# Kernel optimization log

Hardware: AMD Instinct MI355X
Metric: run time of the kernel (lower is better)

The kernel has to match this reference:

```python
import jax, jax.numpy as jnp
import numpy as np

N = 100000       # nodes
E = 1600000      # edges (avg degree 16)
F_IN = 20        # NUM_FEATURES
H = 128          # hidden_channels
EPS = 1e-5       # GraphNorm eps


def setup_inputs() -> dict:
    key = jax.random.key(0)
    ks = jax.random.split(key, 24)
    s = 0.05
    inp = {
        "x": jax.random.normal(ks[0], (N, F_IN), jnp.float32),
        "edge_index": jax.random.randint(ks[1], (2, E), 0, N, dtype=jnp.int32),
    }
    # SAGEConv params: lin_l (neighbors, with bias), lin_r (root, no bias)
    dims = [(F_IN, H), (H, H), (H, H)]
    k = 2
    for i, (din, dout) in enumerate(dims):
        inp[f"Wl{i}"] = jax.random.normal(ks[k], (dout, din), jnp.float32) * s; k += 1
        inp[f"bl{i}"] = jnp.zeros((dout,), jnp.float32)
        inp[f"Wr{i}"] = jax.random.normal(ks[k], (dout, din), jnp.float32) * s; k += 1
        # GraphNorm: weight, bias, mean_scale (alpha)
        inp[f"gw{i}"] = jnp.ones((dout,), jnp.float32)
        inp[f"gb{i}"] = jnp.zeros((dout,), jnp.float32)
        inp[f"ga{i}"] = jnp.ones((dout,), jnp.float32)
    # MLP head: 128 -> 64 -> 32 -> 1
    inp["hW1"] = jax.random.normal(ks[k], (64, H), jnp.float32) * s; k += 1
    inp["hb1"] = jnp.zeros((64,), jnp.float32)
    inp["hW2"] = jax.random.normal(ks[k], (32, 64), jnp.float32) * s; k += 1
    inp["hb2"] = jnp.zeros((32,), jnp.float32)
    inp["hW3"] = jax.random.normal(ks[k], (1, 32), jnp.float32) * s; k += 1
    inp["hb3"] = jnp.zeros((1,), jnp.float32)
    return inp


def _sage(x, src, dst, Wl, bl, Wr):
    # mean aggregation of source features at destination nodes
    deg = jax.ops.segment_sum(jnp.ones((src.shape[0],), x.dtype), dst, num_segments=N)
    agg = jax.ops.segment_sum(x[src], dst, num_segments=N)
    agg = agg / jnp.maximum(deg, 1.0)[:, None]
    return agg @ Wl.T + bl + x @ Wr.T


def _graphnorm(x, w, b, a):
    # single graph (batch=None): stats over all nodes, per channel
    mean = jnp.mean(x, axis=0)
    c = x - a * mean
    var = jnp.mean(c * c, axis=0)
    return w * c * jax.lax.rsqrt(var + EPS) + b


def reference(x, edge_index,
              Wl0, bl0, Wr0, gw0, gb0, ga0,
              Wl1, bl1, Wr1, gw1, gb1, ga1,
              Wl2, bl2, Wr2, gw2, gb2, ga2,
              hW1, hb1, hW2, hb2, hW3, hb3):
    src, dst = edge_index[0], edge_index[1]
    layers = [(Wl0, bl0, Wr0, gw0, gb0, ga0),
              (Wl1, bl1, Wr1, gw1, gb1, ga1),
              (Wl2, bl2, Wr2, gw2, gb2, ga2)]
    h = x
    for (Wl, bl, Wr, gw, gb, ga) in layers:
        h = _sage(h, src, dst, Wl, bl, Wr)
        h = _graphnorm(h, gw, gb, ga)
        h = jax.nn.gelu(h, approximate=False)  # dropout: eval mode (identity)
    h = jax.nn.gelu(h @ hW1.T + hb1, approximate=False)
    h = jax.nn.gelu(h @ hW2.T + hb2, approximate=False)
    out = jax.nn.sigmoid(h @ hW3.T + hb3)
    return out.squeeze(-1)  # [N]
```

## Files before the change

### kernel.cpp

```cpp
#include <hip/hip_runtime.h>
#include <hip/hip_bf16.h>
#include <math.h>

#define NN 100000
#define EE 1600000
#define FIN 20
#define HH 128
#define NBUK 391
#define FILLB 196
#define MMB 782

typedef __attribute__((ext_vector_type(8))) short bf16x8;
typedef __attribute__((ext_vector_type(4))) float f32x4;

__device__ __forceinline__ unsigned short f2b(float x) {
    unsigned int b = __float_as_uint(x);
    unsigned int r = b + 0x7fffu + ((b >> 16) & 1u);
    return (unsigned short)(r >> 16);
}
__device__ __forceinline__ float lof(unsigned int u) { return __uint_as_float(u << 16); }
__device__ __forceinline__ float hif(unsigned int u) { return __uint_as_float(u & 0xffff0000u); }
__device__ __forceinline__ unsigned int pk2(float a, float b) {
    return (unsigned int)f2b(a) | ((unsigned int)f2b(b) << 16);
}

__device__ __forceinline__ float gelu_exact(float z) {
    return 0.5f * z * (1.0f + erff(z * 0.70710678118654752f));
}

__global__ __launch_bounds__(256) void kb_cnt(const int* __restrict__ dst,
                                              int* __restrict__ bcnt) {
    __shared__ int c[NBUK];
    int t = threadIdx.x;
    for (int i = t; i < NBUK; i += 256) c[i] = 0;
    __syncthreads();
    int e0 = blockIdx.x * 8192;
    #pragma unroll 4
    for (int i = 0; i < 32; ++i) {
        int e = e0 + i * 256 + t;
        if (e < EE) atomicAdd(&c[dst[e] >> 8], 1);
    }
    __syncthreads();
    for (int i = t; i < NBUK; i += 256) if (c[i]) atomicAdd(&bcnt[i], c[i]);
}

__global__ void kb_scan(const int* __restrict__ bcnt, int* __restrict__ bbase,
                        int* __restrict__ cursor) {
    __shared__ int sh[512];
    int t = threadIdx.x;
    int v = (t < NBUK) ? bcnt[t] : 0;
    sh[t] = v;
    __syncthreads();
    for (int off = 1; off < 512; off <<= 1) {
        int add = (t >= off) ? sh[t - off] : 0;
        __syncthreads();
        sh[t] += add;
        __syncthreads();
    }
    if (t < NBUK) {
        int ex = sh[t] - v;
        bbase[t] = ex;
        cursor[t] = ex;
    }
    if (t == NBUK - 1) bbase[NBUK] = sh[t];
}

__global__ __launch_bounds__(256) void kb_fill(const int* __restrict__ src,
        const int* __restrict__ dst, int* __restrict__ cursor,
        unsigned int* __restrict__ pairs) {
    __shared__ int cnt[NBUK], base[NBUK], boff[NBUK];
    int t = threadIdx.x;
    for (int i = t; i < NBUK; i += 256) { cnt[i] = 0; boff[i] = 0; }
    __syncthreads();
    int e0 = blockIdx.x * 8192;
    #pragma unroll 4
    for (int i = 0; i < 32; ++i) {
        int e = e0 + i * 256 + t;
        if (e < EE) atomicAdd(&cnt[dst[e] >> 8], 1);
    }
    __syncthreads();
    for (int i = t; i < NBUK; i += 256)
        if (cnt[i]) base[i] = atomicAdd(&cursor[i], cnt[i]);
    __syncthreads();
    #pragma unroll 4
    for (int i = 0; i < 32; ++i) {
        int e = e0 + i * 256 + t;
        if (e < EE) {
            int d = dst[e];
            int b = d >> 8;
            int pos = base[b] + atomicAdd(&boff[b], 1);
            pairs[pos] = (unsigned int)src[e] | ((unsigned int)(d & 255) << 17);
        }
    }
}

__global__ __launch_bounds__(256) void kb_csr(const unsigned int* __restrict__ pairs,
        const int* __restrict__ bbase, int* __restrict__ row_start,
        int* __restrict__ deg, float* __restrict__ invdeg, int* __restrict__ col) {
    __shared__ int ldeg[256];
    __shared__ int lcnt[256];
    int b = blockIdx.x, t = threadIdx.x;
    int e0 = bbase[b], e1 = bbase[b + 1];
    ldeg[t] = 0;
    lcnt[t] = 0;
    __syncthreads();
    for (int e = e0 + t; e < e1; e += 256) atomicAdd(&ldeg[pairs[e] >> 17], 1);
    __syncthreads();
    int d = ldeg[t];
    for (int off = 1; off < 256; off <<= 1) {
        int add = (t >= off) ? ldeg[t - off] : 0;
        __syncthreads();
        ldeg[t] += add;
        __syncthreads();
    }
    int n = b * 256 + t;
    if (n < NN) {
        row_start[n] = e0 + ldeg[t] - d;
        deg[n] = d;
        invdeg[n] = 1.0f / fmaxf((float)d, 1.0f);
    }
    __syncthreads();
    for (int e = e0 + t; e < e1; e += 256) {
        unsigned int p = pairs[e];
        int dL = p >> 17;
        int pos = e0 + (dL ? ldeg[dL - 1] : 0) + atomicAdd(&lcnt[dL], 1);
        col[pos] = (int)(p & 0x1FFFFu);
    }
}

#define XB_N  (NN * 32)
#define A0_N  (NN * 64)
#define PACK_TOTAL (XB_N + A0_N + 8192 + 32768 + 32768 + 8192 + 2048 + 64 + 32 + NBUK)
__global__ __launch_bounds__(256) void k_pack_all(const float* __restrict__ x,
        const float* __restrict__ Wl0, const float* __restrict__ Wr0,
        const float* __restrict__ Wl1, const float* __restrict__ Wr1,
        const float* __restrict__ Wl2, const float* __restrict__ Wr2,
        const float* __restrict__ hW1, const float* __restrict__ hW2,
        const float* __restrict__ hb1, const float* __restrict__ hb2,
        unsigned short* __restrict__ xb, unsigned short* __restrict__ A0,
        unsigned short* __restrict__ Wt0, unsigned short* __restrict__ Wt2a,
        unsigned short* __restrict__ Wt2b, unsigned short* __restrict__ W1b,
        unsigned short* __restrict__ W2b, float* __restrict__ bH1,
        float* __restrict__ bH2, int* __restrict__ bcnt) {
    int id = blockIdx.x * 256 + threadIdx.x;
    if (id < XB_N) {
        int n = id >> 5, k = id & 31;
        xb[id] = f2b((k < FIN) ? x[n * FIN + k] : 0.0f);
        return;
    }
    id -= XB_N;
    if (id < A0_N) {
        int k = id & 63;
        if (k >= FIN) {
            int n = id >> 6;
            float v = (k >= 32 && k < 32 + FIN) ? x[n * FIN + (k - 32)] : 0.0f;
            A0[id] = f2b(v);
        }
        return;
    }
    id -= A0_N;
    if (id < 8192) {
        int c = id >> 6, k = id & 63;
        float v = 0.0f;
        if (k < FIN) v = Wl0[c * FIN + k];
        else if (k >= 32 && k < 32 + FIN) v = Wr0[c * FIN + (k - 32)];
        Wt0[id] = f2b(v);
        return;
    }
    id -= 8192;
    if (id < 32768) {
        int c = id >> 8, k = id & 255;
        Wt2a[id] = f2b((k < HH) ? Wl1[c * HH + k] : Wr1[c * HH + (k - HH)]);
        return;
    }
    id -= 32768;
    if (id < 32768) {
        int c = id >> 8, k = id & 255;
        Wt2b[id] = f2b((k < HH) ? Wl2[c * HH + k] : Wr2[c * HH + (k - HH)]);
        return;
    }
    id -= 32768;
    if (id < 8192) { W1b[id] = f2b(hW1[id]); return; }
    id -= 8192;
    if (id < 2048) { W2b[id] = f2b(hW2[id]); return; }
    id -= 2048;
    if (id < 64) { bH1[id] = hb1[id]; return; }
    id -= 64;
    if (id < 32) { bH2[id] = hb2[id]; return; }
    id -= 32;
    if (id < NBUK) { bcnt[id] = 0; return; }
}

__global__ __launch_bounds__(256) void k_agg0(const uint2* __restrict__ xb2,
        const int* __restrict__ rs, const int* __restrict__ deg,
        const float* __restrict__ inv, const int* __restrict__ col,
        unsigned short* __restrict__ A0) {
    int wid = threadIdx.x >> 6;
    int lane = threadIdx.x & 63;
    int er = lane >> 3;
    int c8 = lane & 7;
    int n = blockIdx.x * 4 + wid;
    if (n >= NN) return;
    int s = rs[n], d = deg[n];
    float a0 = 0.f, a1 = 0.f, a2 = 0.f, a3 = 0.f;
    for (int j0 = 0; j0 < d; j0 += 8) {
        int j = j0 + er;
        if (j < d) {
            int c = col[s + j];
            uint2 v = xb2[(size_t)c * 8 + c8];
            a0 += lof(v.x); a1 += hif(v.x);
            a2 += lof(v.y); a3 += hif(v.y);
        }
    }
    #pragma unroll
    for (int m = 8; m < 64; m <<= 1) {
        a0 += __shfl_xor(a0, m, 64);
        a1 += __shfl_xor(a1, m, 64);
        a2 += __shfl_xor(a2, m, 64);
        a3 += __shfl_xor(a3, m, 64);
    }
    if (er == 0 && c8 < 5) {
        float iv = inv[n];
        uint2 o;
        o.x = pk2(a0 * iv, a1 * iv);
        o.y = pk2(a2 * iv, a3 * iv);
        ((uint2*)A0)[(size_t)n * 16 + c8] = o;
    }
}

__global__ __launch_bounds__(64) void k_aggb(const unsigned short* __restrict__ hB,
        const int* __restrict__ rs, const int* __restrict__ deg,
        const float* __restrict__ inv, const int* __restrict__ col,
        unsigned short* __restrict__ aggB) {
    int n = blockIdx.x;
    int t = threadIdx.x;
    int s = rs[n], d = deg[n];
    const unsigned int* h32 = (const unsigned int*)hB;
    float a0 = 0.0f, a1 = 0.0f;
    int j = 0;
    for (; j + 3 < d; j += 4) {
        int c0 = col[s + j], c1 = col[s + j + 1];
        int c2 = col[s + j + 2], c3 = col[s + j + 3];
        unsigned int u0 = h32[(size_t)c0 * 64 + t];
        unsigned int u1 = h32[(size_t)c1 * 64 + t];
        unsigned int u2 = h32[(size_t)c2 * 64 + t];
        unsigned int u3 = h32[(size_t)c3 * 64 + t];
        a0 += lof(u0) + lof(u1) + lof(u2) + lof(u3);
        a1 += hif(u0) + hif(u1) + hif(u2) + hif(u3);
    }
    for (; j < d; ++j) {
        unsigned int u = h32[(size_t)col[s + j] * 64 + t];
        a0 += lof(u);
        a1 += hif(u);
    }
    float iv = inv[n];
    ((unsigned int*)aggB)[(size_t)n * 64 + t] = pk2(a0 * iv, a1 * iv);
}

__global__ __launch_bounds__(256) void k_mm(const unsigned short* __restrict__ A0,
        const unsigned short* __restrict__ A1, int c0, int kChunks, int lda,
        const unsigned short* __restrict__ B, int ldb,
        const float* __restrict__ bias, unsigned short* __restrict__ outB,
        float* __restrict__ psPart, float* __restrict__ pqPart, int M) {
    __shared__ __align__(16) unsigned short As[128 * 40];
    __shared__ __align__(16) unsigned short Bs[128 * 40];
    __shared__ float redS[2][128], redQ[2][128];
    const int tid = threadIdx.x;
    const int m0 = blockIdx.x * 128;
    const int w = tid >> 6, lane = tid & 63;
    const int wr = w >> 1, wc = w & 1;
    const int m16 = lane & 15, q = lane >> 4;

    f32x4 acc[4][4];
    #pragma unroll
    for (int i = 0; i < 4; ++i)
        #pragma unroll
        for (int j = 0; j < 4; ++j) acc[i][j] = (f32x4){0.f, 0.f, 0.f, 0.f};

    for (int chunk = 0; chunk < kChunks; ++chunk) {
        const unsigned short* A = (chunk < c0) ? A0 : A1;
        const int kb = (chunk - ((chunk < c0) ? 0 : c0)) * 32;
        #pragma unroll
        for (int it = 0; it < 2; ++it) {
            int s = tid + it * 256;
            int r = s >> 2, p = s & 3;
            int gm = m0 + r;
            uint4 v = make_uint4(0u, 0u, 0u, 0u);
            if (gm < M) v = *(const uint4*)(A + (size_t)gm * lda + kb + p * 8);
            *(uint4*)&As[r * 40 + p * 8] = v;
        }
        {
            const int kbB = chunk * 32;
            #pragma unroll
            for (int it = 0; it < 2; ++it) {
                int s = tid + it * 256;
                int r = s >> 2, p = s & 3;
                uint4 v = *(const uint4*)(B + (size_t)r * ldb + kbB + p * 8);
                *(uint4*)&Bs[r * 40 + p * 8] = v;
            }
        }
        __syncthreads();
        bf16x8 af[4], bfr[4];
        #pragma unroll
        for (int i = 0; i < 4; ++i)
            af[i] = *(const bf16x8*)&As[(wr * 64 + i * 16 + m16) * 40 + q * 8];
        #pragma unroll
        for (int j = 0; j < 4; ++j)
            bfr[j] = *(const bf16x8*)&Bs[(wc * 64 + j * 16 + m16) * 40 + q * 8];
        #pragma unroll
        for (int i = 0; i < 4; ++i)
            #pragma unroll
            for (int j = 0; j < 4; ++j)
                acc[i][j] = __builtin_amdgcn_mfma_f32_16x16x32_bf16(af[i], bfr[j], acc[i][j], 0, 0, 0);
        __syncthreads();
    }

    float cs[4] = {0.f, 0.f, 0.f, 0.f};
    float cq[4] = {0.f, 0.f, 0.f, 0.f};
    #pragma unroll
    for (int i = 0; i < 4; ++i) {
        int mBase = m0 + wr * 64 + i * 16 + q * 4;
        #pragma unroll
        for (int j = 0; j < 4; ++j) {
            int cc = wc * 64 + j * 16 + m16;
            float bv = bias[cc];
            #pragma unroll
            for (int r = 0; r < 4; ++r) {
                int m = mBase + r;
                float v = (m < M) ? (acc[i][j][r] + bv) : 0.0f;
                if (m < M) outB[(size_t)m * 128 + cc] = f2b(v);
                cs[j] += v;
                cq[j] += v * v;
            }
        }
    }
    #pragma unroll
    for (int msk = 16; msk < 64; msk <<= 1) {
        #pragma unroll
        for (int j = 0; j < 4; ++j) {
            cs[j] += __shfl_xor(cs[j], msk, 64);
            cq[j] += __shfl_xor(cq[j], msk, 64);
        }
    }
    if (q == 0) {
        #pragma unroll
        for (int j = 0; j < 4; ++j) {
            int cc = wc * 64 + j * 16 + m16;
            redS[wr][cc] = cs[j];
            redQ[wr][cc] = cq[j];
        }
    }
    __syncthreads();
    if (tid < 128) {
        psPart[(size_t)blockIdx.x * 128 + tid] = redS[0][tid] + redS[1][tid];
        pqPart[(size_t)blockIdx.x * 128 + tid] = redQ[0][tid] + redQ[1][tid];
    }
}

__global__ __launch_bounds__(1024) void k_gn_final(const float* __restrict__ ps,
        const float* __restrict__ pq, const float* __restrict__ gw,
        const float* __restrict__ gb, const float* __restrict__ ga,
        float* __restrict__ cA, float* __restrict__ cB, int nP) {
    __shared__ float shs[8][128], shq[8][128];
    int c = threadIdx.x & 127, sl = threadIdx.x >> 7;
    float s = 0.0f, q = 0.0f;
    for (int b = sl; b < nP; b += 8) {
        s += ps[b * 128 + c];
        q += pq[b * 128 + c];
    }
    shs[sl][c] = s;
    shq[sl][c] = q;
    __syncthreads();
    if (threadIdx.x < 128) {
        float S = 0.0f, Q = 0.0f;
        #pragma unroll
        for (int i = 0; i < 8; ++i) { S += shs[i][c]; Q += shq[i][c]; }
        float mean = S / (float)NN;
        float msq  = Q / (float)NN;
        float a = ga[c];
        float var = msq - mean * mean * a * (2.0f - a);
        float rstd = rsqrtf(var + 1e-5f);
        float A = gw[c] * rstd;
        cA[c] = A;
        cB[c] = gb[c] - a * mean * A;
    }
}

__global__ __launch_bounds__(256) void k_gn_apply(const unsigned short* __restrict__ yB,
        const float* __restrict__ cA, const float* __restrict__ cB,
        unsigned short* __restrict__ hB) {
    int i = blockIdx.x * 256 + threadIdx.x;
    if (i >= NN * 16) return;
    int g = i & 15;
    uint4 v = ((const uint4*)yB)[i];
    float4 A0 = ((const float4*)cA)[g * 2];
    float4 A1 = ((const float4*)cA)[g * 2 + 1];
    float4 B0 = ((const float4*)cB)[g * 2];
    float4 B1 = ((const float4*)cB)[g * 2 + 1];
    unsigned int o0 = pk2(gelu_exact(lof(v.x) * A0.x + B0.x),
                          gelu_exact(hif(v.x) * A0.y + B0.y));
    unsigned int o1 = pk2(gelu_exact(lof(v.y) * A0.z + B0.z),
                          gelu_exact(hif(v.y) * A0.w + B0.w));
    unsigned int o2 = pk2(gelu_exact(lof(v.z) * A1.x + B1.x),
                          gelu_exact(hif(v.z) * A1.y + B1.y));
    unsigned int o3 = pk2(gelu_exact(lof(v.w) * A1.z + B1.z),
                          gelu_exact(hif(v.w) * A1.w + B1.w));
    ((uint4*)hB)[i] = make_uint4(o0, o1, o2, o3);
}

__global__ __launch_bounds__(256) void k_headf(const unsigned short* __restrict__ yB,
        const float* __restrict__ cAp, const float* __restrict__ cBp,
        const unsigned short* __restrict__ W1b, const float* __restrict__ b1,
        const unsigned short* __restrict__ W2b, const float* __restrict__ b2,
        const float* __restrict__ W3, const float* __restrict__ b3,
        float* __restrict__ out) {
    __shared__ __align__(16) char pool[23040];
    unsigned short* As  = (unsigned short*)pool;
    unsigned short* Bs  = (unsigned short*)(pool + 10240);
    unsigned short* As2 = (unsigned short*)pool;
    unsigned short* Bs2 = (unsigned short*)(pool + 18432);
    const int tid = threadIdx.x;
    const int m0 = blockIdx.x * 128;
    const int w = tid >> 6, lane = tid & 63;
    const int m16 = lane & 15, q = lane >> 4;
    const float4* cA4 = (const float4*)cAp;
    const float4* cB4 = (const float4*)cBp;

    #pragma unroll
    for (int it = 0; it < 8; ++it) {
        int i = tid + it * 256;
        if (i < 2048) Bs2[(i >> 6) * 72 + (i & 63)] = W2b[i];
    }

    f32x4 acc1[2][4];
    #pragma unroll
    for (int i = 0; i < 2; ++i)
        #pragma unroll
        for (int j = 0; j < 4; ++j) acc1[i][j] = (f32x4){0.f, 0.f, 0.f, 0.f};

    for (int chunk = 0; chunk < 4; ++chunk) {
        const int kb = chunk * 32;
        #pragma unroll
        for (int it = 0; it < 2; ++it) {
            int s = tid + it * 256;
            int r = s >> 2, p = s & 3;
            int gm = m0 + r;
            uint4 v = make_uint4(0u, 0u, 0u, 0u);
            if (gm < NN) v = *(const uint4*)(yB + (size_t)gm * 128 + kb + p * 8);
            int cg = chunk * 8 + p * 2;
            float4 Ax = cA4[cg], Ay = cA4[cg + 1];
            float4 Bx = cB4[cg], By = cB4[cg + 1];
            uint4 o;
            o.x = pk2(gelu_exact(lof(v.x) * Ax.x + Bx.x),
                      gelu_exact(hif(v.x) * Ax.y + Bx.y));
            o.y = pk2(gelu_exact(lof(v.y) * Ax.z + Bx.z),
                      gelu_exact(hif(v.y) * Ax.w + Bx.w));
            o.z = pk2(gelu_exact(lof(v.z) * Ay.x + By.x),
                      gelu_exact(hif(v.z) * Ay.y + By.y));
            o.w = pk2(gelu_exact(lof(v.w) * Ay.z + By.z),
                      gelu_exact(hif(v.w) * Ay.w + By.w));
            *(uint4*)&As[r * 40 + p * 8] = o;
        }
        {
            int r = tid >> 2, p = tid & 3;
            uint4 v = *(const uint4*)(W1b + (size_t)r * 128 + kb + p * 8);
            *(uint4*)&Bs[r * 40 + p * 8] = v;
        }
        __syncthreads();
        bf16x8 af[2], bfr[4];
        #pragma unroll
        for (int i = 0; i < 2; ++i)
            af[i] = *(const bf16x8*)&As[(w * 32 + i * 16 + m16) * 40 + q * 8];
        #pragma unroll
        for (int j = 0; j < 4; ++j)
            bfr[j] = *(const bf16x8*)&Bs[(j * 16 + m16) * 40 + q * 8];
        #pragma unroll
        for (int i = 0; i < 2; ++i)
            #pragma unroll
            for (int j = 0; j < 4; ++j)
                acc1[i][j] = __builtin_amdgcn_mfma_f32_16x16x32_bf16(af[i], bfr[j], acc1[i][j], 0, 0, 0);
        __syncthreads();
    }

    {
        float b1v[4];
        #pragma unroll
        for (int j = 0; j < 4; ++j) b1v[j] = b1[j * 16 + m16];
        #pragma unroll
        for (int i = 0; i < 2; ++i) {
            int mloc = w * 32 + i * 16 + q * 4;
            #pragma unroll
            for (int j = 0; j < 4; ++j) {
                int c = j * 16 + m16;
                #pragma unroll
                for (int r = 0; r < 4; ++r)
                    As2[(mloc + r) * 72 + c] = f2b(gelu_exact(acc1[i][j][r] + b1v[j]));
            }
        }
    }
    __syncthreads();

    f32x4 acc2[2][2];
    #pragma unroll
    for (int i = 0; i < 2; ++i)
        #pragma unroll
        for (int j = 0; j < 2; ++j) acc2[i][j] = (f32x4){0.f, 0.f, 0.f, 0.f};
    #pragma unroll
    for (int kc = 0; kc < 2; ++kc) {
        bf16x8 a2[2], bf2[2];
        #pragma unroll
        for (int i = 0; i < 2; ++i)
            a2[i] = *(const bf16x8*)&As2[(w * 32 + i * 16 + m16) * 72 + kc * 32 + q * 8];
        #pragma unroll
        for (int j = 0; j < 2; ++j)
            bf2[j] = *(const bf16x8*)&Bs2[(j * 16 + m16) * 72 + kc * 32 + q * 8];
        #pragma unroll
        for (int i = 0; i < 2; ++i)
            #pragma unroll
            for (int j = 0; j < 2; ++j)
                acc2[i][j] = __builtin_amdgcn_mfma_f32_16x16x32_bf16(a2[i], bf2[j], acc2[i][j], 0, 0, 0);
    }

    float w3a = W3[m16], w3b = W3[16 + m16];
    float b2a = b2[m16], b2b = b2[16 + m16];
    float p[8];
    #pragma unroll
    for (int i = 0; i < 2; ++i)
        #pragma unroll
        for (int r = 0; r < 4; ++r) {
            float za = gelu_exact(acc2[i][0][r] + b2a);
            float zb = gelu_exact(acc2[i][1][r] + b2b);
            p[i * 4 + r] = za * w3a + zb * w3b;
        }
    #pragma unroll
    for (int msk = 1; msk < 16; msk <<= 1)
        #pragma unroll
        for (int k = 0; k < 8; ++k) p[k] += __shfl_xor(p[k], msk, 64);
    if (m16 == 0) {
        float b3v = b3[0];
        #pragma unroll
        for (int i = 0; i < 2; ++i)
            #pragma unroll
            for (int r = 0; r < 4; ++r) {
                int m = m0 + w * 32 + i * 16 + q * 4 + r;
                if (m < NN) out[m] = 1.0f / (1.0f + expf(-(p[i * 4 + r] + b3v)));
            }
    }
}

extern "C" void kernel_launch(void* const* d_in, const int* in_sizes, int n_in,
                              void* d_out, int out_size, void* d_ws, size_t ws_size,
                              hipStream_t stream) {
    const float* x   = (const float*)d_in[0];
    const int*   ei  = (const int*)d_in[1];
    const float* Wl0 = (const float*)d_in[2];
    const float* bl0 = (const float*)d_in[3];
    const float* Wr0 = (const float*)d_in[4];
    const float* gw0 = (const float*)d_in[5];
    const float* gb0 = (const float*)d_in[6];
    const float* ga0 = (const float*)d_in[7];
    const float* Wl1 = (const float*)d_in[8];
    const float* bl1 = (const float*)d_in[9];
    const float* Wr1 = (const float*)d_in[10];
    const float* gw1 = (const float*)d_in[11];
    const float* gb1 = (const float*)d_in[12];
    const float* ga1 = (const float*)d_in[13];
    const float* Wl2 = (const float*)d_in[14];
    const float* bl2 = (const float*)d_in[15];
    const float* Wr2 = (const float*)d_in[16];
    const float* gw2 = (const float*)d_in[17];
    const float* gb2 = (const float*)d_in[18];
    const float* ga2 = (const float*)d_in[19];
    const float* hW1 = (const float*)d_in[20];
    const float* hb1 = (const float*)d_in[21];
    const float* hW2 = (const float*)d_in[22];
    const float* hb2 = (const float*)d_in[23];
    const float* hW3 = (const float*)d_in[24];
    const float* hb3 = (const float*)d_in[25];
    float* out = (float*)d_out;

    size_t off = 0;
    auto carve = [&](size_t bytes) -> void* {
        void* p = (void*)((char*)d_ws + off);
        off += (bytes + 255) & ~(size_t)255;
        return p;
    };
    int*   bcnt      = (int*)carve((size_t)NBUK * 4);
    int*   bbase     = (int*)carve((size_t)(NBUK + 1) * 4);
    int*   cursor    = (int*)carve((size_t)NBUK * 4);
    unsigned int* pairs = (unsigned int*)carve((size_t)EE * 4);
    int*   deg       = (int*)carve((size_t)NN * 4);
    int*   row_start = (int*)carve((size_t)NN * 4);
    float* invdeg    = (float*)carve((size_t)NN * 4);
    int*   colarr    = (int*)carve((size_t)EE * 4);
    unsigned short* xb    = (unsigned short*)carve((size_t)NN * 32 * 2);
    unsigned short* Wt0   = (unsigned short*)carve(128 * 64 * 2);
    unsigned short* Wt2a  = (unsigned short*)carve(128 * 256 * 2);
    unsigned short* Wt2b  = (unsigned short*)carve(128 * 256 * 2);
    unsigned short* W1b   = (unsigned short*)carve(64 * 128 * 2);
    unsigned short* W2b   = (unsigned short*)carve(32 * 64 * 2);
    float* biasH1    = (float*)carve(64 * 4);
    float* biasH2    = (float*)carve(32 * 4);
    float* ps        = (float*)carve((size_t)MMB * 128 * 4);
    float* pq        = (float*)carve((size_t)MMB * 128 * 4);
    float* cAall     = (float*)carve(3 * 128 * 4);
    float* cBall     = (float*)carve(3 * 128 * 4);
    unsigned short* A0pack = (unsigned short*)carve((size_t)NN * 64 * 2);
    unsigned short* hB   = (unsigned short*)carve((size_t)NN * HH * 2);
    unsigned short* aggB = (unsigned short*)carve((size_t)NN * HH * 2);
    unsigned short* yB   = (unsigned short*)carve((size_t)NN * HH * 2);
    if (off > ws_size) return;

    const int* src = ei;
    const int* dst = ei + EE;

    k_pack_all<<<(PACK_TOTAL + 255) / 256, 256, 0, stream>>>(
        x, Wl0, Wr0, Wl1, Wr1, Wl2, Wr2, hW1, hW2, hb1, hb2,
        xb, A0pack, Wt0, Wt2a, Wt2b, W1b, W2b, biasH1, biasH2, bcnt);
    kb_cnt<<<FILLB, 256, 0, stream>>>(dst, bcnt);
    kb_scan<<<1, 512, 0, stream>>>(bcnt, bbase, cursor);
    kb_fill<<<FILLB, 256, 0, stream>>>(src, dst, cursor, pairs);
    kb_csr<<<NBUK, 256, 0, stream>>>(pairs, bbase, row_start, deg, invdeg, colarr);

    k_agg0<<<(NN + 3) / 4, 256, 0, stream>>>((const uint2*)xb, row_start,
                                             deg, invdeg, colarr, A0pack);
    k_mm<<<MMB, 256, 0, stream>>>(A0pack, A0pack, 2, 2, 64, Wt0, 64, bl0, yB, ps, pq, NN);
    k_gn_final<<<1, 1024, 0, stream>>>(ps, pq, gw0, gb0, ga0, cAall + 0, cBall + 0, MMB);
    k_gn_apply<<<(NN * 16 + 255) / 256, 256, 0, stream>>>(yB, cAall + 0, cBall + 0, hB);

    k_aggb<<<NN, 64, 0, stream>>>(hB, row_start, deg, invdeg, colarr, aggB);
    k_mm<<<MMB, 256, 0, stream>>>(aggB, hB, 4, 8, 128, Wt2a, 256, bl1, yB, ps, pq, NN);
    k_gn_final<<<1, 1024, 0, stream>>>(ps, pq, gw1, gb1, ga1, cAall + 128, cBall + 128, MMB);
    k_gn_apply<<<(NN * 16 + 255) / 256, 256, 0, stream>>>(yB, cAall + 128, cBall + 128, hB);

    k_aggb<<<NN, 64, 0, stream>>>(hB, row_start, deg, invdeg, colarr, aggB);
    k_mm<<<MMB, 256, 0, stream>>>(aggB, hB, 4, 8, 128, Wt2b, 256, bl2, yB, ps, pq, NN);
    k_gn_final<<<1, 1024, 0, stream>>>(ps, pq, gw2, gb2, ga2, cAall + 256, cBall + 256, MMB);

    k_headf<<<MMB, 256, 0, stream>>>(yB, cAall + 256, cBall + 256,
                                     W1b, biasH1, W2b, biasH2, hW3, hb3, out);
}
```

Before: 555.4 us.

## Fuse neighbor mean-aggregation into the SAGE matmul kernels via shared-memory A tile

Result: slower. 989.4 us (+78.1%).

```diff
diff --git a/kernel.cpp b/kernel.cpp
--- a/kernel.cpp
+++ b/kernel.cpp
@@ -129,15 +129,14 @@
 }
 
 #define XB_N  (NN * 32)
-#define A0_N  (NN * 64)
-#define PACK_TOTAL (XB_N + A0_N + 8192 + 32768 + 32768 + 8192 + 2048 + 64 + 32 + NBUK)
+#define PACK_TOTAL (XB_N + 8192 + 32768 + 32768 + 8192 + 2048 + 64 + 32 + NBUK)
 __global__ __launch_bounds__(256) void k_pack_all(const float* __restrict__ x,
         const float* __restrict__ Wl0, const float* __restrict__ Wr0,
         const float* __restrict__ Wl1, const float* __restrict__ Wr1,
         const float* __restrict__ Wl2, const float* __restrict__ Wr2,
         const float* __restrict__ hW1, const float* __restrict__ hW2,
         const float* __restrict__ hb1, const float* __restrict__ hb2,
-        unsigned short* __restrict__ xb, unsigned short* __restrict__ A0,
+        unsigned short* __restrict__ xb,
         unsigned short* __restrict__ Wt0, unsigned short* __restrict__ Wt2a,
         unsigned short* __restrict__ Wt2b, unsigned short* __restrict__ W1b,
         unsigned short* __restrict__ W2b, float* __restrict__ bH1,
@@ -149,16 +148,6 @@
         return;
     }
     id -= XB_N;
-    if (id < A0_N) {
-        int k = id & 63;
-        if (k >= FIN) {
-            int n = id >> 6;
-            float v = (k >= 32 && k < 32 + FIN) ? x[n * FIN + (k - 32)] : 0.0f;
-            A0[id] = f2b(v);
-        }
-        return;
-    }
-    id -= A0_N;
     if (id < 8192) {
         int c = id >> 6, k = id & 63;
         float v = 0.0f;
@@ -191,77 +180,136 @@
     if (id < NBUK) { bcnt[id] = 0; return; }
 }
 
-__global__ __launch_bounds__(256) void k_agg0(const uint2* __restrict__ xb2,
+__global__ __launch_bounds__(256) void k_mm0(const uint2* __restrict__ xb2,
         const int* __restrict__ rs, const int* __restrict__ deg,
         const float* __restrict__ inv, const int* __restrict__ col,
-        unsigned short* __restrict__ A0) {
-    int wid = threadIdx.x >> 6;
-    int lane = threadIdx.x & 63;
-    int er = lane >> 3;
-    int c8 = lane & 7;
-    int n = blockIdx.x * 4 + wid;
-    if (n >= NN) return;
-    int s = rs[n], d = deg[n];
-    float a0 = 0.f, a1 = 0.f, a2 = 0.f, a3 = 0.f;
-    for (int j0 = 0; j0 < d; j0 += 8) {
-        int j = j0 + er;
-        if (j < d) {
-            int c = col[s + j];
-            uint2 v = xb2[(size_t)c * 8 + c8];
-            a0 += lof(v.x); a1 += hif(v.x);
-            a2 += lof(v.y); a3 += hif(v.y);
-        }
-    }
-    #pragma unroll
-    for (int m = 8; m < 64; m <<= 1) {
-        a0 += __shfl_xor(a0, m, 64);
-        a1 += __shfl_xor(a1, m, 64);
-        a2 += __shfl_xor(a2, m, 64);
-        a3 += __shfl_xor(a3, m, 64);
-    }
-    if (er == 0 && c8 < 5) {
-        float iv = inv[n];
-        uint2 o;
-        o.x = pk2(a0 * iv, a1 * iv);
-        o.y = pk2(a2 * iv, a3 * iv);
-        ((uint2*)A0)[(size_t)n * 16 + c8] = o;
-    }
-}
-
-__global__ __launch_bounds__(64) void k_aggb(const unsigned short* __restrict__ hB,
+        const unsigned short* __restrict__ B, const float* __restrict__ bias,
+        unsigned short* __restrict__ outB, float* __restrict__ psPart,
+        float* __restrict__ pqPart, int M) {
+    __shared__ __align__(16) unsigned short Ag[128 * 72];
+    __shared__ __align__(16) unsigned short Bs[128 * 40];
+    __shared__ float redS[2][128], redQ[2][128];
+    const int tid = threadIdx.x;
+    const int m0 = blockIdx.x * 128;
+    const int w = tid >> 6, lane = tid & 63;
+    const int wr = w >> 1, wc = w & 1;
+    const int m16 = lane & 15, q = lane >> 4;
+    const int er = lane >> 3, c8 = lane & 7;
+
+    for (int nn = w; nn < 128; nn += 4) {
+        int n = m0 + nn;
+        float a0 = 0.f, a1 = 0.f, a2 = 0.f, a3 = 0.f;
+        if (n < M) {
+            int s = rs[n], d = deg[n];
+            for (int j0 = 0; j0 < d; j0 += 8) {
+                int j = j0 + er;
+                if (j < d) {
+                    int c = col[s + j];
+                    uint2 v = xb2[(size_t)c * 8 + c8];
+                    a0 += lof(v.x); a1 += hif(v.x);
+                    a2 += lof(v.y); a3 += hif(v.y);
+                }
+            }
+            #pragma unroll
+            for (int m = 8; m < 64; m <<= 1) {
+                a0 += __shfl_xor(a0, m, 64);
+                a1 += __shfl_xor(a1, m, 64);
+                a2 += __shfl_xor(a2, m, 64);
+                a3 += __shfl_xor(a3, m, 64);
+            }
+        }
+        if (er == 0) {
+            float iv = (n < M) ? inv[n] : 0.0f;
+            uint2 o = make_uint2(0u, 0u);
+            if (c8 < 5) { o.x = pk2(a0 * iv, a1 * iv); o.y = pk2(a2 * iv, a3 * iv); }
+            *(uint2*)&Ag[nn * 72 + c8 * 4] = o;
+        } else if (er == 1) {
+            uint2 v = make_uint2(0u, 0u);
+            if (n < M) v = xb2[(size_t)n * 8 + c8];
+            *(uint2*)&Ag[nn * 72 + 32 + c8 * 4] = v;
+        }
+    }
+
+    f32x4 acc[4][4];
+    #pragma unroll
+    for (int i = 0; i < 4; ++i)
+        #pragma unroll
+        for (int j = 0; j < 4; ++j) acc[i][j] = (f32x4){0.f, 0.f, 0.f, 0.f};
+
+    for (int chunk = 0; chunk < 2; ++chunk) {
+        const int kb = chunk * 32;
+        #pragma unroll
+        for (int it = 0; it < 2; ++it) {
+            int s = tid + it * 256;
+            int r = s >> 2, p = s & 3;
+            uint4 v = *(const uint4*)(B + (size_t)r * 64 + kb + p * 8);
+            *(uint4*)&Bs[r * 40 + p * 8] = v;
+        }
+        __syncthreads();
+        bf16x8 af[4], bfr[4];
+        #pragma unroll
+        for (int i = 0; i < 4; ++i)
+            af[i] = *(const bf16x8*)&Ag[(wr * 64 + i * 16 + m16) * 72 + kb + q * 8];
+        #pragma unroll
+        for (int j = 0; j < 4; ++j)
+            bfr[j] = *(const bf16x8*)&Bs[(wc * 64 + j * 16 + m16) * 40 + q * 8];
+        #pragma unroll
+        for (int i = 0; i < 4; ++i)
+            #pragma unroll
+            for (int j = 0; j < 4; ++j)
+                acc[i][j] = __builtin_amdgcn_mfma_f32_16x16x32_bf16(af[i], bfr[j], acc[i][j], 0, 0, 0);
+        __syncthreads();
+    }
+
+    float cs[4] = {0.f, 0.f, 0.f, 0.f};
+    float cq[4] = {0.f, 0.f, 0.f, 0.f};
+    #pragma unroll
+    for (int i = 0; i < 4; ++i) {
+        int mBase = m0 + wr * 64 + i * 16 + q * 4;
+        #pragma unroll
+        for (int j = 0; j < 4; ++j) {
+            int cc = wc * 64 + j * 16 + m16;
+            float bv = bias[cc];
+            #pragma unroll
+            for (int r = 0; r < 4; ++r) {
+                int m = mBase + r;
+                float v = (m < M) ? (acc[i][j][r] + bv) : 0.0f;
+                if (m < M) outB[(size_t)m * 128 + cc] = f2b(v);
+                cs[j] += v;
+                cq[j] += v * v;
+            }
+        }
+    }
+    #pragma unroll
+    for (int msk = 16; msk < 64; msk <<= 1) {
+        #pragma unroll
+        for (int j = 0; j < 4; ++j) {
+            cs[j] += __shfl_xor(cs[j], msk, 64);
+            cq[j] += __shfl_xor(cq[j], msk, 64);
+        }
+    }
+    if (q == 0) {
+        #pragma unroll
+        for (int j = 0; j < 4; ++j) {
+            int cc = wc * 64 + j * 16 + m16;
+            redS[wr][cc] = cs[j];
+            redQ[wr][cc] = cq[j];
+        }
+    }
+    __syncthreads();
+    if (tid < 128) {
+        psPart[(size_t)blockIdx.x * 128 + tid] = redS[0][tid] + redS[1][tid];
+        pqPart[(size_t)blockIdx.x * 128 + tid] = redQ[0][tid] + redQ[1][tid];
+    }
+}
+
+__global__ __launch_bounds__(256) void k_mmagg(const unsigned short* __restrict__ hB,
         const int* __restrict__ rs, const int* __restrict__ deg,
         const float* __restrict__ inv, const int* __restrict__ col,
-        unsigned short* __restrict__ aggB) {
-    int n = blockIdx.x;
-    int t = threadIdx.x;
-    int s = rs[n], d = deg[n];
-    const unsigned int* h32 = (const unsigned int*)hB;
-    float a0 = 0.0f, a1 = 0.0f;
-    int j = 0;
-    for (; j + 3 < d; j += 4) {
-        int c0 = col[s + j], c1 = col[s + j + 1];
-        int c2 = col[s + j + 2], c3 = col[s + j + 3];
-        unsigned int u0 = h32[(size_t)c0 * 64 + t];
-        unsigned int u1 = h32[(size_t)c1 * 64 + t];
-        unsigned int u2 = h32[(size_t)c2 * 64 + t];
-        unsigned int u3 = h32[(size_t)c3 * 64 + t];
-        a0 += lof(u0) + lof(u1) + lof(u2) + lof(u3);
-        a1 += hif(u0) + hif(u1) + hif(u2) + hif(u3);
-    }
-    for (; j < d; ++j) {
-        unsigned int u = h32[(size_t)col[s + j] * 64 + t];
-        a0 += lof(u);
-        a1 += hif(u);
-    }
-    float iv = inv[n];
-    ((unsigned int*)aggB)[(size_t)n * 64 + t] = pk2(a0 * iv, a1 * iv);
-}
-
-__global__ __launch_bounds__(256) void k_mm(const unsigned short* __restrict__ A0,
-        const unsigned short* __restrict__ A1, int c0, int kChunks, int lda,
-        const unsigned short* __restrict__ B, int ldb,
-        const float* __restrict__ bias, unsigned short* __restrict__ outB,
-        float* __restrict__ psPart, float* __restrict__ pqPart, int M) {
+        const unsigned short* __restrict__ B, const float* __restrict__ bias,
+        unsigned short* __restrict__ outB, float* __restrict__ psPart,
+        float* __restrict__ pqPart, int M) {
+    __shared__ __align__(16) unsigned short Ag[128 * 136];
     __shared__ __align__(16) unsigned short As[128 * 40];
     __shared__ __align__(16) unsigned short Bs[128 * 40];
     __shared__ float redS[2][128], redQ[2][128];
@@ -270,6 +318,43 @@
     const int w = tid >> 6, lane = tid & 63;
     const int wr = w >> 1, wc = w & 1;
     const int m16 = lane & 15, q = lane >> 4;
+    const unsigned int* h32 = (const unsigned int*)hB;
+
+    for (int nn = w; nn < 128; nn += 4) {
+        int n = m0 + nn;
+        float a0 = 0.0f, a1 = 0.0f;
+        float iv = 0.0f;
+        if (n < M) {
+            int s = rs[n], d = deg[n];
+            int j = 0;
+            for (; j + 7 < d; j += 8) {
+                int c0 = col[s + j],     c1 = col[s + j + 1];
+                int c2 = col[s + j + 2], c3 = col[s + j + 3];
+                int c4 = col[s + j + 4], c5 = col[s + j + 5];
+                int c6 = col[s + j + 6], c7 = col[s + j + 7];
+                unsigned int u0 = h32[(size_t)c0 * 64 + lane];
+                unsigned int u1 = h32[(size_t)c1 * 64 + lane];
+                unsigned int u2 = h32[(size_t)c2 * 64 + lane];
+                unsigned int u3 = h32[(size_t)c3 * 64 + lane];
+                unsigned int u4 = h32[(size_t)c4 * 64 + lane];
+                unsigned int u5 = h32[(size_t)c5 * 64 + lane];
+                unsigned int u6 = h32[(size_t)c6 * 64 + lane];
+                unsigned int u7 = h32[(size_t)c7 * 64 + lane];
+                a0 += lof(u0) + lof(u1) + lof(u2) + lof(u3)
+                    + lof(u4) + lof(u5) + lof(u6) + lof(u7);
+                a1 += hif(u0) + hif(u1) + hif(u2) + hif(u3)
+                    + hif(u4) + hif(u5) + hif(u6) + hif(u7);
+            }
+            for (; j < d; ++j) {
+                unsigned int u = h32[(size_t)col[s + j] * 64 + lane];
+                a0 += lof(u);
+                a1 += hif(u);
+            }
+            iv = inv[n];
+        }
+        *(unsigned int*)&Ag[nn * 136 + lane * 2] = pk2(a0 * iv, a1 * iv);
+    }
+    __syncthreads();
 
     f32x4 acc[4][4];
     #pragma unroll
@@ -277,33 +362,40 @@
         #pragma unroll
         for (int j = 0; j < 4; ++j) acc[i][j] = (f32x4){0.f, 0.f, 0.f, 0.f};
 
-    for (int chunk = 0; chunk < kChunks; ++chunk) {
-        const unsigned short* A = (chunk < c0) ? A0 : A1;
-        const int kb = (chunk - ((chunk < c0) ? 0 : c0)) * 32;
-        #pragma unroll
-        for (int it = 0; it < 2; ++it) {
-            int s = tid + it * 256;
-            int r = s >> 2, p = s & 3;
-            int gm = m0 + r;
-            uint4 v = make_uint4(0u, 0u, 0u, 0u);
-            if (gm < M) v = *(const uint4*)(A + (size_t)gm * lda + kb + p * 8);
-            *(uint4*)&As[r * 40 + p * 8] = v;
-        }
-        {
-            const int kbB = chunk * 32;
+    for (int chunk = 0; chunk < 8; ++chunk) {
+        if (chunk >= 4) {
+            const int kb = (chunk - 4) * 32;
             #pragma unroll
             for (int it = 0; it < 2; ++it) {
                 int s = tid + it * 256;
                 int r = s >> 2, p = s & 3;
-                uint4 v = *(const uint4*)(B + (size_t)r * ldb + kbB + p * 8);
+                int gm = m0 + r;
+                uint4 v = make_uint4(0u, 0u, 0u, 0u);
+                if (gm < M) v = *(const uint4*)(hB + (size_t)gm * 128 + kb + p * 8);
+                *(uint4*)&As[r * 40 + p * 8] = v;
+            }
+        }
+        {
+            const int kbB = chunk * 32;
+            #pragma unroll
+            for (int it = 0; it < 2; ++it) {
+                int s = tid + it * 256;
+                int r = s >> 2, p = s & 3;
+                uint4 v = *(const uint4*)(B + (size_t)r * 256 + kbB + p * 8);
                 *(uint4*)&Bs[r * 40 + p * 8] = v;
             }
         }
         __syncthreads();
         bf16x8 af[4], bfr[4];
-        #pragma unroll
-        for (int i = 0; i < 4; ++i)
-            af[i] = *(const bf16x8*)&As[(wr * 64 + i * 16 + m16) * 40 + q * 8];
+        if (chunk < 4) {
+            #pragma unroll
+            for (int i = 0; i < 4; ++i)
+                af[i] = *(const bf16x8*)&Ag[(wr * 64 + i * 16 + m16) * 136 + chunk * 32 + q * 8];
+        } else {
+            #pragma unroll
+            for (int i = 0; i < 4; ++i)
+                af[i] = *(const bf16x8*)&As[(wr * 64 + i * 16 + m16) * 40 + q * 8];
+        }
         #pragma unroll
         for (int j = 0; j < 4; ++j)
             bfr[j] = *(const bf16x8*)&Bs[(wc * 64 + j * 16 + m16) * 40 + q * 8];
@@ -605,9 +697,7 @@
     float* pq        = (float*)carve((size_t)MMB * 128 * 4);
     float* cAall     = (float*)carve(3 * 128 * 4);
     float* cBall     = (float*)carve(3 * 128 * 4);
-    unsigned short* A0pack = (unsigned short*)carve((size_t)NN * 64 * 2);
     unsigned short* hB   = (unsigned short*)carve((size_t)NN * HH * 2);
-    unsigned short* aggB = (unsigned short*)carve((size_t)NN * HH * 2);
     unsigned short* yB   = (unsigned short*)carve((size_t)NN * HH * 2);
     if (off > ws_size) return;
 
@@ -616,25 +706,24 @@
 
     k_pack_all<<<(PACK_TOTAL + 255) / 256, 256, 0, stream>>>(
         x, Wl0, Wr0, Wl1, Wr1, Wl2, Wr2, hW1, hW2, hb1, hb2,
-        xb, A0pack, Wt0, Wt2a, Wt2b, W1b, W2b, biasH1, biasH2, bcnt);
+        xb, Wt0, Wt2a, Wt2b, W1b, W2b, biasH1, biasH2, bcnt);
     kb_cnt<<<FILLB, 256, 0, stream>>>(dst, bcnt);
     kb_scan<<<1, 512, 0, stream>>>(bcnt, bbase, cursor);
     kb_fill<<<FILLB, 256, 0, stream>>>(src, dst, cursor, pairs);
     kb_csr<<<NBUK, 256, 0, stream>>>(pairs, bbase, row_start, deg, invdeg, colarr);
 
-    k_agg0<<<(NN + 3) / 4, 256, 0, stream>>>((const uint2*)xb, row_start,
-                                             deg, invdeg, colarr, A0pack);
-    k_mm<<<MMB, 256, 0, stream>>>(A0pack, A0pack, 2, 2, 64, Wt0, 64, bl0, yB, ps, pq, NN);
+    k_mm0<<<MMB, 256, 0, stream>>>((const uint2*)xb, row_start, deg, invdeg,
+                                   colarr, Wt0, bl0, yB, ps, pq, NN);
     k_gn_final<<<1, 1024, 0, stream>>>(ps, pq, gw0, gb0, ga0, cAall + 0, cBall + 0, MMB);
     k_gn_apply<<<(NN * 16 + 255) / 256, 256, 0, stream>>>(yB, cAall + 0, cBall + 0, hB);
 
-    k_aggb<<<NN, 64, 0, stream>>>(hB, row_start, deg, invdeg, colarr, aggB);
-    k_mm<<<MMB, 256, 0, stream>>>(aggB, hB, 4, 8, 128, Wt2a, 256, bl1, yB, ps, pq, NN);
+    k_mmagg<<<MMB, 256, 0, stream>>>(hB, row_start, deg, invdeg, colarr,
+                                     Wt2a, bl1, yB, ps, pq, NN);
     k_gn_final<<<1, 1024, 0, stream>>>(ps, pq, gw1, gb1, ga1, cAall + 128, cBall + 128, MMB);
     k_gn_apply<<<(NN * 16 + 255) / 256, 256, 0, stream>>>(yB, cAall + 128, cBall + 128, hB);
 
-    k_aggb<<<NN, 64, 0, stream>>>(hB, row_start, deg, invdeg, colarr, aggB);
-    k_mm<<<MMB, 256, 0, stream>>>(aggB, hB, 4, 8, 128, Wt2b, 256, bl2, yB, ps, pq, NN);
+    k_mmagg<<<MMB, 256, 0, stream>>>(hB, row_start, deg, invdeg, colarr,
+                                     Wt2b, bl2, yB, ps, pq, NN);
     k_gn_final<<<1, 1024, 0, stream>>>(ps, pq, gw2, gb2, ga2, cAall + 256, cBall + 256, MMB);
 
     k_headf<<<MMB, 256, 0, stream>>>(yB, cAall + 256, cBall + 256,
```

## Replace bucket count/scan with fixed-capacity buckets and stage CSR columns in LDS

Applied to the files above, without the earlier changes.

Result: no change. 546.4 us (-1.6%).

```diff
diff --git a/kernel.cpp b/kernel.cpp
--- a/kernel.cpp
+++ b/kernel.cpp
@@ -9,6 +9,7 @@
 #define NBUK 391
 #define FILLB 196
 #define MMB 782
+#define CAP 6144
 
 typedef __attribute__((ext_vector_type(8))) short bf16x8;
 typedef __attribute__((ext_vector_type(4))) float f32x4;
@@ -26,43 +27,6 @@
 
 __device__ __forceinline__ float gelu_exact(float z) {
     return 0.5f * z * (1.0f + erff(z * 0.70710678118654752f));
-}
-
-__global__ __launch_bounds__(256) void kb_cnt(const int* __restrict__ dst,
-                                              int* __restrict__ bcnt) {
-    __shared__ int c[NBUK];
-    int t = threadIdx.x;
-    for (int i = t; i < NBUK; i += 256) c[i] = 0;
-    __syncthreads();
-    int e0 = blockIdx.x * 8192;
-    #pragma unroll 4
-    for (int i = 0; i < 32; ++i) {
-        int e = e0 + i * 256 + t;
-        if (e < EE) atomicAdd(&c[dst[e] >> 8], 1);
-    }
-    __syncthreads();
-    for (int i = t; i < NBUK; i += 256) if (c[i]) atomicAdd(&bcnt[i], c[i]);
-}
-
-__global__ void kb_scan(const int* __restrict__ bcnt, int* __restrict__ bbase,
-                        int* __restrict__ cursor) {
-    __shared__ int sh[512];
-    int t = threadIdx.x;
-    int v = (t < NBUK) ? bcnt[t] : 0;
-    sh[t] = v;
-    __syncthreads();
-    for (int off = 1; off < 512; off <<= 1) {
-        int add = (t >= off) ? sh[t - off] : 0;
-        __syncthreads();
-        sh[t] += add;
-        __syncthreads();
-    }
-    if (t < NBUK) {
-        int ex = sh[t] - v;
-        bbase[t] = ex;
-        cursor[t] = ex;
-    }
-    if (t == NBUK - 1) bbase[NBUK] = sh[t];
 }
 
 __global__ __launch_bounds__(256) void kb_fill(const int* __restrict__ src,
@@ -89,22 +53,25 @@
             int d = dst[e];
             int b = d >> 8;
             int pos = base[b] + atomicAdd(&boff[b], 1);
-            pairs[pos] = (unsigned int)src[e] | ((unsigned int)(d & 255) << 17);
+            pairs[(size_t)b * CAP + pos] = (unsigned int)src[e]
+                                         | ((unsigned int)(d & 255) << 17);
         }
     }
 }
 
 __global__ __launch_bounds__(256) void kb_csr(const unsigned int* __restrict__ pairs,
-        const int* __restrict__ bbase, int* __restrict__ row_start,
+        const int* __restrict__ cursor, int* __restrict__ row_start,
         int* __restrict__ deg, float* __restrict__ invdeg, int* __restrict__ col) {
     __shared__ int ldeg[256];
     __shared__ int lcnt[256];
+    __shared__ int colL[CAP];
     int b = blockIdx.x, t = threadIdx.x;
-    int e0 = bbase[b], e1 = bbase[b + 1];
+    int e0 = b * CAP;
+    int cb = cursor[b];
     ldeg[t] = 0;
     lcnt[t] = 0;
     __syncthreads();
-    for (int e = e0 + t; e < e1; e += 256) atomicAdd(&ldeg[pairs[e] >> 17], 1);
+    for (int e = t; e < cb; e += 256) atomicAdd(&ldeg[pairs[e0 + e] >> 17], 1);
     __syncthreads();
     int d = ldeg[t];
     for (int off = 1; off < 256; off <<= 1) {
@@ -120,12 +87,14 @@
         invdeg[n] = 1.0f / fmaxf((float)d, 1.0f);
     }
     __syncthreads();
-    for (int e = e0 + t; e < e1; e += 256) {
-        unsigned int p = pairs[e];
+    for (int e = t; e < cb; e += 256) {
+        unsigned int p = pairs[e0 + e];
         int dL = p >> 17;
-        int pos = e0 + (dL ? ldeg[dL - 1] : 0) + atomicAdd(&lcnt[dL], 1);
-        col[pos] = (int)(p & 0x1FFFFu);
-    }
+        int pos = (dL ? ldeg[dL - 1] : 0) + atomicAdd(&lcnt[dL], 1);
+        colL[pos] = (int)(p & 0x1FFFFu);
+    }
+    __syncthreads();
+    for (int e = t; e < cb; e += 256) col[e0 + e] = colL[e];
 }
 
 #define XB_N  (NN * 32)
@@ -141,7 +110,7 @@
         unsigned short* __restrict__ Wt0, unsigned short* __restrict__ Wt2a,
         unsigned short* __restrict__ Wt2b, unsigned short* __restrict__ W1b,
         unsigned short* __restrict__ W2b, float* __restrict__ bH1,
-        float* __restrict__ bH2, int* __restrict__ bcnt) {
+        float* __restrict__ bH2, int* __restrict__ cursor) {
     int id = blockIdx.x * 256 + threadIdx.x;
     if (id < XB_N) {
         int n = id >> 5, k = id & 31;
@@ -188,7 +157,7 @@
     id -= 64;
     if (id < 32) { bH2[id] = hb2[id]; return; }
     id -= 32;
-    if (id < NBUK) { bcnt[id] = 0; return; }
+    if (id < NBUK) { cursor[id] = 0; return; }
 }
 
 __global__ __launch_bounds__(256) void k_agg0(const uint2* __restrict__ xb2,
@@ -585,14 +554,12 @@
         off += (bytes + 255) & ~(size_t)255;
         return p;
     };
-    int*   bcnt      = (int*)carve((size_t)NBUK * 4);
-    int*   bbase     = (int*)carve((size_t)(NBUK + 1) * 4);
     int*   cursor    = (int*)carve((size_t)NBUK * 4);
-    unsigned int* pairs = (unsigned int*)carve((size_t)EE * 4);
+    unsigned int* pairs = (unsigned int*)carve((size_t)NBUK * CAP * 4);
     int*   deg       = (int*)carve((size_t)NN * 4);
     int*   row_start = (int*)carve((size_t)NN * 4);
     float* invdeg    = (float*)carve((size_t)NN * 4);
-    int*   colarr    = (int*)carve((size_t)EE * 4);
+    int*   colarr    = (int*)carve((size_t)NBUK * CAP * 4);
     unsigned short* xb    = (unsigned short*)carve((size_t)NN * 32 * 2);
     unsigned short* Wt0   = (unsigned short*)carve(128 * 64 * 2);
     unsigned short* Wt2a  = (unsigned short*)carve(128 * 256 * 2);
@@ -616,11 +583,9 @@
 
     k_pack_all<<<(PACK_TOTAL + 255) / 256, 256, 0, stream>>>(
         x, Wl0, Wr0, Wl1, Wr1, Wl2, Wr2, hW1, hW2, hb1, hb2,
-        xb, A0pack, Wt0, Wt2a, Wt2b, W1b, W2b, biasH1, biasH2, bcnt);
-    kb_cnt<<<FILLB, 256, 0, stream>>>(dst, bcnt);
-    kb_scan<<<1, 512, 0, stream>>>(bcnt, bbase, cursor);
+        xb, A0pack, Wt0, Wt2a, Wt2b, W1b, W2b, biasH1, biasH2, cursor);
     kb_fill<<<FILLB, 256, 0, stream>>>(src, dst, cursor, pairs);
-    kb_csr<<<NBUK, 256, 0, stream>>>(pairs, bbase, row_start, deg, invdeg, colarr);
+    kb_csr<<<NBUK, 256, 0, stream>>>(pairs, cursor, row_start, deg, invdeg, colarr);
 
     k_agg0<<<(NN + 3) / 4, 256, 0, stream>>>((const uint2*)xb, row_start,
                                              deg, invdeg, colarr, A0pack);
```
